# Performance work log

Hardware: AMD Instinct MI355X
Metric: run time of the kernel (lower is better)

The kernel has to match this reference:

```python
import jax, jax.numpy as jnp
import numpy as np

EPS = 1e-5  # torch LayerNorm default


def _lstm_layer(x, Wih, Whh, bih, bhh):
    """Batched multi-weight LSTM layer.
    x: (N, T, I); Wih: (N, 4H, I); Whh: (N, 4H, H); bih, bhh: (N, 4H).
    Gate order matches PyTorch: i, f, g, o.
    Returns (hs: (N, T, H), h_last: (N, H)).
    """
    N, T, _ = x.shape
    H = Whh.shape[-1]
    # Precompute input projections for all timesteps (high-intensity GEMM).
    xW = jnp.einsum('nti,ngi->ntg', x, Wih) + (bih + bhh)[:, None, :]  # (N, T, 4H)

    def step(carry, xt):
        h, c = carry
        gates = xt + jnp.einsum('nh,ngh->ng', h, Whh)  # (N, 4H)
        i, f, g, o = jnp.split(gates, 4, axis=-1)
        i = jax.nn.sigmoid(i)
        f = jax.nn.sigmoid(f)
        g = jnp.tanh(g)
        o = jax.nn.sigmoid(o)
        c = f * c + i * g
        h = o * jnp.tanh(c)
        return (h, c), h

    h0 = jnp.zeros((N, H), dtype=x.dtype)
    c0 = jnp.zeros((N, H), dtype=x.dtype)
    (h_last, _), hs = jax.lax.scan(step, (h0, c0), jnp.swapaxes(xW, 0, 1))
    return jnp.swapaxes(hs, 0, 1), h_last


def _layer_norm(x, gamma, beta):
    mu = jnp.mean(x, axis=-1, keepdims=True)
    var = jnp.mean(jnp.square(x - mu), axis=-1, keepdims=True)
    return (x - mu) * jax.lax.rsqrt(var + EPS) * gamma + beta


def setup_inputs() -> dict:
    key = jax.random.key(0)
    N, T, I, H = 128, 512, 32, 256
    ks = jax.random.split(key, 10)
    k = 1.0 / np.sqrt(H)  # torch LSTM init scale
    u = lambda kk, shape: jax.random.uniform(kk, shape, jnp.float32, -k, k)
    return {
        'x': jax.random.normal(ks[0], (N, T, I), jnp.float32),
        # layer 0 (input I -> H)
        'Wih0': u(ks[1], (N, 4 * H, I)),
        'Whh0': u(ks[2], (N, 4 * H, H)),
        'bih0': u(ks[3], (N, 4 * H)),
        'bhh0': u(ks[4], (N, 4 * H)),
        # layer 1 (H -> H)
        'Wih1': u(ks[5], (N, 4 * H, H)),
        'Whh1': u(ks[6], (N, 4 * H, H)),
        'bih1': u(ks[7], (N, 4 * H)),
        'bhh1': u(ks[8], (N, 4 * H)),
        # LayerNorm params
        'gamma': jnp.ones((H,), jnp.float32),
        'beta': jnp.zeros((H,), jnp.float32),
    }


def reference(x, Wih0, Whh0, bih0, bhh0, Wih1, Whh1, bih1, bhh1, gamma, beta):
    # Eval-mode forward: Dropout layers are identity.
    hs0, _ = _lstm_layer(x, Wih0, Whh0, bih0, bhh0)      # (N, T, H)
    _, h_last = _lstm_layer(hs0, Wih1, Whh1, bih1, bhh1)  # (N, H) = top-layer final hidden state
    return _layer_norm(h_last, gamma, beta)               # (N, H)
```

## Files before the change

kernel.cpp:

```cpp
#include <hip/hip_runtime.h>
#include <hip/hip_bf16.h>


typedef _Float16 half2_t __attribute__((ext_vector_type(2)));
typedef _Float16 half8_t __attribute__((ext_vector_type(8)));
typedef float floatx4 __attribute__((ext_vector_type(4)));

__device__ __forceinline__ unsigned pk(float a, float b) {
  half2_t h = { (_Float16)a, (_Float16)b };
  return __builtin_bit_cast(unsigned, h);
}
__device__ __forceinline__ float fdot2(unsigned w, unsigned h, float c) {
  return __builtin_amdgcn_fdot2(__builtin_bit_cast(half2_t, w),
                                __builtin_bit_cast(half2_t, h), c, false);
}
__device__ __forceinline__ float h2f(unsigned short u) {
  return (float)__builtin_bit_cast(_Float16, u);
}
__device__ __forceinline__ unsigned short f2h(float f) {
  return __builtin_bit_cast(unsigned short, (_Float16)f);
}
__device__ __forceinline__ float sigmf(float x) {
  return __builtin_amdgcn_rcpf(1.f + __expf(-x));
}
__device__ __forceinline__ float tanh_(float x) {
  return 2.f * sigmf(2.f * x) - 1.f;
}
__device__ __forceinline__ floatx4 mfma16(half8_t a, half8_t b, floatx4 c) {
  return __builtin_amdgcn_mfma_f32_16x16x32_f16(a, b, c, 0, 0, 0);
}

template<int K, int KT, bool AF16>
__global__ __launch_bounds__(256)
void gemm_xw(const void* __restrict__ Ap, const float* __restrict__ Bp,
             unsigned short* __restrict__ Cp)
{
  __shared__ unsigned short As[128][KT + 8];
  __shared__ unsigned short Bs[128][KT + 8];
  const int tid = threadIdx.x;
  const int node = blockIdx.y;
  const int mt = blockIdx.x >> 3;
  const int nt = blockIdx.x & 7;
  const int lane = tid & 63, wv = tid >> 6;
  const int wr = wv >> 1, wc = wv & 1;
  const int lm = lane & 15, lk = (lane >> 4) * 8;

  floatx4 zero = {0.f, 0.f, 0.f, 0.f};
  floatx4 acc[4][4];
#pragma unroll
  for (int i = 0; i < 4; ++i)
#pragma unroll
    for (int j = 0; j < 4; ++j) acc[i][j] = zero;

  for (int kt = 0; kt < K; kt += KT) {
    if (AF16) {
      const unsigned short* A = (const unsigned short*)Ap + (size_t)node * 512 * K;
      const int CPR = KT / 8;
#pragma unroll
      for (int c = tid; c < 128 * CPR; c += 256) {
        int r = c / CPR, cc = (c % CPR) * 8;
        *(uint4*)&As[r][cc] =
            *(const uint4*)(A + (size_t)(mt * 128 + r) * K + kt + cc);
      }
    } else {
      const float* A = (const float*)Ap + (size_t)node * 512 * K;
      const int CPR = KT / 4;
#pragma unroll
      for (int c = tid; c < 128 * CPR; c += 256) {
        int r = c / CPR, cc = (c % CPR) * 4;
        float4 v = *(const float4*)(A + (size_t)(mt * 128 + r) * K + kt + cc);
        uint2 p = make_uint2(pk(v.x, v.y), pk(v.z, v.w));
        *(uint2*)&As[r][cc] = p;
      }
    }
    {
      const float* B = Bp + (size_t)node * 1024 * K;
      const int CPR = KT / 4;
#pragma unroll
      for (int c = tid; c < 128 * CPR; c += 256) {
        int r = c / CPR, cc = (c % CPR) * 4;
        float4 v = *(const float4*)(B + (size_t)(nt * 128 + r) * K + kt + cc);
        uint2 p = make_uint2(pk(v.x, v.y), pk(v.z, v.w));
        *(uint2*)&Bs[r][cc] = p;
      }
    }
    __syncthreads();
#pragma unroll
    for (int ks = 0; ks < KT / 32; ++ks) {
      half8_t af[4], bf[4];
#pragma unroll
      for (int i = 0; i < 4; ++i)
        af[i] = *(const half8_t*)&As[wr * 64 + i * 16 + lm][ks * 32 + lk];
#pragma unroll
      for (int j = 0; j < 4; ++j)
        bf[j] = *(const half8_t*)&Bs[wc * 64 + j * 16 + lm][ks * 32 + lk];
#pragma unroll
      for (int i = 0; i < 4; ++i)
#pragma unroll
        for (int j = 0; j < 4; ++j)
          acc[i][j] = mfma16(af[i], bf[j], acc[i][j]);
    }
    __syncthreads();
  }
  unsigned short* C = Cp + (size_t)node * 512 * 1024;
#pragma unroll
  for (int i = 0; i < 4; ++i)
#pragma unroll
    for (int j = 0; j < 4; ++j)
#pragma unroll
      for (int r = 0; r < 4; ++r) {
        int row = mt * 128 + wr * 64 + i * 16 + (lane >> 4) * 4 + r;
        int col = nt * 128 + wc * 64 + j * 16 + lm;
        C[(size_t)row * 1024 + col] = f2h(acc[i][j][r]);
      }
}

#define VWP 96

template<bool WRITE_HS, bool FINAL>
__global__ __launch_bounds__(512, 2)
void lstm_rec(const unsigned short* __restrict__ xW,
              const float* __restrict__ Whh,
              const float* __restrict__ bih, const float* __restrict__ bhh,
              unsigned* __restrict__ hs,
              const float* __restrict__ gamma, const float* __restrict__ beta,
              float* __restrict__ out)
{
  __shared__ uint4 lw4[16][512];
  __shared__ __align__(16) unsigned short hbuf[256];
  __shared__ float fBuf[256], oBuf[256];
  __shared__ float redBuf[2];

  const int tid = threadIdx.x;
  const int n = blockIdx.x;
  const int g0 = tid, g1 = tid + 512;

  const float b0 = bih[n * 1024 + g0] + bhh[n * 1024 + g0];
  const float b1 = bih[n * 1024 + g1] + bhh[n * 1024 + g1];

  const float4* w0p = (const float4*)(Whh + ((size_t)n * 1024 + g0) * 256);
  const float4* w1p = (const float4*)(Whh + ((size_t)n * 1024 + g1) * 256);
  unsigned wv0[VWP], wv1[VWP];
#pragma unroll
  for (int i = 0; i < VWP / 2; ++i) {
    float4 v = w0p[i];
    wv0[2 * i] = pk(v.x, v.y);
    wv0[2 * i + 1] = pk(v.z, v.w);
    float4 u = w1p[i];
    wv1[2 * i] = pk(u.x, u.y);
    wv1[2 * i + 1] = pk(u.z, u.w);
  }
#pragma unroll
  for (int i = 0; i < 8; ++i) {
    float4 a = w0p[48 + 2 * i], b = w0p[49 + 2 * i];
    lw4[i][tid] = make_uint4(pk(a.x, a.y), pk(a.z, a.w), pk(b.x, b.y), pk(b.z, b.w));
    float4 c4 = w1p[48 + 2 * i], d4 = w1p[49 + 2 * i];
    lw4[8 + i][tid] = make_uint4(pk(c4.x, c4.y), pk(c4.z, c4.w), pk(d4.x, d4.y), pk(d4.z, d4.w));
  }

  if (tid < 32) ((uint4*)hbuf)[tid] = make_uint4(0, 0, 0, 0);
  float c = 0.f, hl = 0.f;
  const unsigned short* xwp = xW + (size_t)n * 512 * 1024;
  __syncthreads();

  for (int t = 0; t < 512; ++t) {
    unsigned short xu0 = xwp[t * 1024 + g0];
    unsigned short xu1 = xwp[t * 1024 + g1];
    float a0 = b0, a1 = b1;
    const uint4* h4 = (const uint4*)hbuf;
#pragma unroll
    for (int q = 0; q < 24; ++q) {
      uint4 hp = h4[q];
      a0 = fdot2(wv0[4 * q + 0], hp.x, a0); a1 = fdot2(wv1[4 * q + 0], hp.x, a1);
      a0 = fdot2(wv0[4 * q + 1], hp.y, a0); a1 = fdot2(wv1[4 * q + 1], hp.y, a1);
      a0 = fdot2(wv0[4 * q + 2], hp.z, a0); a1 = fdot2(wv1[4 * q + 2], hp.z, a1);
      a0 = fdot2(wv0[4 * q + 3], hp.w, a0); a1 = fdot2(wv1[4 * q + 3], hp.w, a1);
    }
#pragma unroll
    for (int q = 0; q < 8; ++q) {
      uint4 hp = h4[24 + q];
      uint4 u0 = lw4[q][tid], u1 = lw4[8 + q][tid];
      a0 = fdot2(u0.x, hp.x, a0); a1 = fdot2(u1.x, hp.x, a1);
      a0 = fdot2(u0.y, hp.y, a0); a1 = fdot2(u1.y, hp.y, a1);
      a0 = fdot2(u0.z, hp.z, a0); a1 = fdot2(u1.z, hp.z, a1);
      a0 = fdot2(u0.w, hp.w, a0); a1 = fdot2(u1.w, hp.w, a1);
    }
    a0 += h2f(xu0);
    a1 += h2f(xu1);

    float iact = 0.f, gact = 0.f;
    if (tid < 256) {
      iact = sigmf(a0);
      gact = tanh_(a1);
    } else {
      fBuf[tid - 256] = sigmf(a0);
      oBuf[tid - 256] = sigmf(a1);
    }
    __syncthreads();
    if (tid < 256) {
      c = fBuf[tid] * c + iact * gact;
      hl = oBuf[tid] * tanh_(c);
      hbuf[tid] = f2h(hl);
    }
    __syncthreads();
    if (WRITE_HS && tid < 128)
      hs[((size_t)n * 512 + t) * 128 + tid] = ((const unsigned*)hbuf)[tid];
  }

  if (FINAL) {
    if (tid < 256) fBuf[tid] = hl;
    __syncthreads();
    if (tid < 64) {
      float s = fBuf[tid] + fBuf[tid + 64] + fBuf[tid + 128] + fBuf[tid + 192];
      for (int off = 32; off > 0; off >>= 1) s += __shfl_down(s, off, 64);
      if (tid == 0) redBuf[0] = s * (1.f / 256.f);
    }
    __syncthreads();
    float mu = redBuf[0];
    if (tid < 256) oBuf[tid] = (hl - mu) * (hl - mu);
    __syncthreads();
    if (tid < 64) {
      float s = oBuf[tid] + oBuf[tid + 64] + oBuf[tid + 128] + oBuf[tid + 192];
      for (int off = 32; off > 0; off >>= 1) s += __shfl_down(s, off, 64);
      if (tid == 0) redBuf[1] = s * (1.f / 256.f);
    }
    __syncthreads();
    if (tid < 256) {
      float var = redBuf[1];
      out[(size_t)n * 256 + tid] =
          (hl - mu) * rsqrtf(var + 1e-5f) * gamma[tid] + beta[tid];
    }
  }
}

extern "C" void kernel_launch(void* const* d_in, const int* in_sizes, int n_in,
                              void* d_out, int out_size, void* d_ws, size_t ws_size,
                              hipStream_t stream) {
  const float* x     = (const float*)d_in[0];
  const float* Wih0  = (const float*)d_in[1];
  const float* Whh0  = (const float*)d_in[2];
  const float* bih0  = (const float*)d_in[3];
  const float* bhh0  = (const float*)d_in[4];
  const float* Wih1  = (const float*)d_in[5];
  const float* Whh1  = (const float*)d_in[6];
  const float* bih1  = (const float*)d_in[7];
  const float* bhh1  = (const float*)d_in[8];
  const float* gamma = (const float*)d_in[9];
  const float* beta  = (const float*)d_in[10];
  float* out = (float*)d_out;

  unsigned short* xw  = (unsigned short*)d_ws;
  unsigned short* hs0 = (unsigned short*)((char*)d_ws + (size_t)134217728);

  gemm_xw<32, 32, false><<<dim3(32, 128), 256, 0, stream>>>(x, Wih0, xw);
  lstm_rec<true, false><<<128, 512, 0, stream>>>(xw, Whh0, bih0, bhh0,
                                                 (unsigned*)hs0, nullptr, nullptr,
                                                 nullptr);
  gemm_xw<256, 128, true><<<dim3(32, 128), 256, 0, stream>>>(hs0, Wih1, xw);
  lstm_rec<false, true><<<128, 512, 0, stream>>>(xw, Whh1, bih1, bhh1, nullptr,
                                                 gamma, beta, out);
}
```

Measured before the change: 2.469 ms.

## Restructure LSTM recurrence: 256 threads, split-K across lane quads with DPP reduction

```diff
diff --git a/kernel.cpp b/kernel.cpp
--- a/kernel.cpp
+++ b/kernel.cpp
@@ -28,6 +28,12 @@
 }
 __device__ __forceinline__ floatx4 mfma16(half8_t a, half8_t b, floatx4 c) {
   return __builtin_amdgcn_mfma_f32_16x16x32_f16(a, b, c, 0, 0, 0);
+}
+template<int CTRL>
+__device__ __forceinline__ float dppf(float x) {
+  return __builtin_bit_cast(
+      float, __builtin_amdgcn_update_dpp(0, __builtin_bit_cast(int, x), CTRL,
+                                         0xf, 0xf, true));
 }
 
 template<int K, int KT, bool AF16>
@@ -115,121 +121,131 @@
       }
 }
 
-#define VWP 96
-
 template<bool WRITE_HS, bool FINAL>
-__global__ __launch_bounds__(512, 2)
+__global__ __launch_bounds__(256, 1)
 void lstm_rec(const unsigned short* __restrict__ xW,
               const float* __restrict__ Whh,
               const float* __restrict__ bih, const float* __restrict__ bhh,
-              unsigned* __restrict__ hs,
+              unsigned short* __restrict__ hs,
               const float* __restrict__ gamma, const float* __restrict__ beta,
               float* __restrict__ out)
 {
-  __shared__ uint4 lw4[16][512];
-  __shared__ __align__(16) unsigned short hbuf[256];
-  __shared__ float fBuf[256], oBuf[256];
-  __shared__ float redBuf[2];
+  __shared__ uint4 lwL[16][2][256];
+  __shared__ __align__(16) unsigned short hbuf[2][256];
+  __shared__ float red[256];
+  __shared__ float redv[2];
 
   const int tid = threadIdx.x;
   const int n = blockIdx.x;
-  const int g0 = tid, g1 = tid + 512;
-
-  const float b0 = bih[n * 1024 + g0] + bhh[n * 1024 + g0];
-  const float b1 = bih[n * 1024 + g1] + bhh[n * 1024 + g1];
-
-  const float4* w0p = (const float4*)(Whh + ((size_t)n * 1024 + g0) * 256);
-  const float4* w1p = (const float4*)(Whh + ((size_t)n * 1024 + g1) * 256);
-  unsigned wv0[VWP], wv1[VWP];
-#pragma unroll
-  for (int i = 0; i < VWP / 2; ++i) {
-    float4 v = w0p[i];
-    wv0[2 * i] = pk(v.x, v.y);
-    wv0[2 * i + 1] = pk(v.z, v.w);
-    float4 u = w1p[i];
-    wv1[2 * i] = pk(u.x, u.y);
-    wv1[2 * i + 1] = pk(u.z, u.w);
-  }
-#pragma unroll
-  for (int i = 0; i < 8; ++i) {
-    float4 a = w0p[48 + 2 * i], b = w0p[49 + 2 * i];
-    lw4[i][tid] = make_uint4(pk(a.x, a.y), pk(a.z, a.w), pk(b.x, b.y), pk(b.z, b.w));
-    float4 c4 = w1p[48 + 2 * i], d4 = w1p[49 + 2 * i];
-    lw4[8 + i][tid] = make_uint4(pk(c4.x, c4.y), pk(c4.z, c4.w), pk(d4.x, d4.y), pk(d4.z, d4.w));
-  }
-
-  if (tid < 32) ((uint4*)hbuf)[tid] = make_uint4(0, 0, 0, 0);
+  const int l = tid & 63, w = tid >> 6;
+  const int r = l & 3;
+  const int u0 = w * 64 + (l >> 2) * 4;
+  const int u = w * 64 + l;
+
+  float bias[4];
+#pragma unroll
+  for (int G = 0; G < 4; ++G)
+    bias[G] = bih[n * 1024 + G * 256 + u] + bhh[n * 1024 + G * 256 + u];
+
+  unsigned wv[16 * 24];
+#pragma unroll
+  for (int G = 0; G < 4; ++G)
+#pragma unroll
+    for (int j = 0; j < 4; ++j) {
+      const int s = G * 4 + j;
+      const int row = G * 256 + u0 + ((r + j) & 3);
+      const float4* Wp =
+          (const float4*)(Whh + ((size_t)n * 1024 + row) * 256 + 64 * r);
+#pragma unroll
+      for (int m = 0; m < 12; ++m) {
+        float4 v = Wp[m];
+        wv[s * 24 + 2 * m]     = pk(v.x, v.y);
+        wv[s * 24 + 2 * m + 1] = pk(v.z, v.w);
+      }
+      float4 a = Wp[12], b = Wp[13];
+      lwL[s][0][tid] = make_uint4(pk(a.x, a.y), pk(a.z, a.w), pk(b.x, b.y), pk(b.z, b.w));
+      float4 c4 = Wp[14], d4 = Wp[15];
+      lwL[s][1][tid] = make_uint4(pk(c4.x, c4.y), pk(c4.z, c4.w), pk(d4.x, d4.y), pk(d4.z, d4.w));
+    }
+
+  hbuf[0][tid] = 0;
   float c = 0.f, hl = 0.f;
   const unsigned short* xwp = xW + (size_t)n * 512 * 1024;
   __syncthreads();
 
   for (int t = 0; t < 512; ++t) {
-    unsigned short xu0 = xwp[t * 1024 + g0];
-    unsigned short xu1 = xwp[t * 1024 + g1];
-    float a0 = b0, a1 = b1;
-    const uint4* h4 = (const uint4*)hbuf;
-#pragma unroll
-    for (int q = 0; q < 24; ++q) {
-      uint4 hp = h4[q];
-      a0 = fdot2(wv0[4 * q + 0], hp.x, a0); a1 = fdot2(wv1[4 * q + 0], hp.x, a1);
-      a0 = fdot2(wv0[4 * q + 1], hp.y, a0); a1 = fdot2(wv1[4 * q + 1], hp.y, a1);
-      a0 = fdot2(wv0[4 * q + 2], hp.z, a0); a1 = fdot2(wv1[4 * q + 2], hp.z, a1);
-      a0 = fdot2(wv0[4 * q + 3], hp.w, a0); a1 = fdot2(wv1[4 * q + 3], hp.w, a1);
-    }
-#pragma unroll
-    for (int q = 0; q < 8; ++q) {
-      uint4 hp = h4[24 + q];
-      uint4 u0 = lw4[q][tid], u1 = lw4[8 + q][tid];
-      a0 = fdot2(u0.x, hp.x, a0); a1 = fdot2(u1.x, hp.x, a1);
-      a0 = fdot2(u0.y, hp.y, a0); a1 = fdot2(u1.y, hp.y, a1);
-      a0 = fdot2(u0.z, hp.z, a0); a1 = fdot2(u1.z, hp.z, a1);
-      a0 = fdot2(u0.w, hp.w, a0); a1 = fdot2(u1.w, hp.w, a1);
-    }
-    a0 += h2f(xu0);
-    a1 += h2f(xu1);
-
-    float iact = 0.f, gact = 0.f;
-    if (tid < 256) {
-      iact = sigmf(a0);
-      gact = tanh_(a1);
-    } else {
-      fBuf[tid - 256] = sigmf(a0);
-      oBuf[tid - 256] = sigmf(a1);
-    }
-    __syncthreads();
-    if (tid < 256) {
-      c = fBuf[tid] * c + iact * gact;
-      hl = oBuf[tid] * tanh_(c);
-      hbuf[tid] = f2h(hl);
-    }
-    __syncthreads();
-    if (WRITE_HS && tid < 128)
-      hs[((size_t)n * 512 + t) * 128 + tid] = ((const unsigned*)hbuf)[tid];
+    const int p = t & 1, np = p ^ 1;
+    unsigned short xv0 = xwp[t * 1024 + 0 * 256 + u];
+    unsigned short xv1 = xwp[t * 1024 + 1 * 256 + u];
+    unsigned short xv2 = xwp[t * 1024 + 2 * 256 + u];
+    unsigned short xv3 = xwp[t * 1024 + 3 * 256 + u];
+
+    unsigned hd[32];
+    {
+      const uint4* hb = (const uint4*)(&hbuf[p][64 * r]);
+#pragma unroll
+      for (int m = 0; m < 8; ++m) {
+        uint4 q = hb[m];
+        hd[4 * m] = q.x; hd[4 * m + 1] = q.y; hd[4 * m + 2] = q.z; hd[4 * m + 3] = q.w;
+      }
+    }
+
+    float acc[16];
+#pragma unroll
+    for (int s = 0; s < 16; ++s) {
+      float a = 0.f;
+#pragma unroll
+      for (int d = 0; d < 24; ++d) a = fdot2(wv[s * 24 + d], hd[d], a);
+      uint4 t0 = lwL[s][0][tid];
+      a = fdot2(t0.x, hd[24], a); a = fdot2(t0.y, hd[25], a);
+      a = fdot2(t0.z, hd[26], a); a = fdot2(t0.w, hd[27], a);
+      uint4 t1 = lwL[s][1][tid];
+      a = fdot2(t1.x, hd[28], a); a = fdot2(t1.y, hd[29], a);
+      a = fdot2(t1.z, hd[30], a); a = fdot2(t1.w, hd[31], a);
+      acc[s] = a;
+    }
+
+    float A0 = acc[0] + dppf<0x93>(acc[1]) + dppf<0x4E>(acc[2]) + dppf<0x39>(acc[3]);
+    float A1 = acc[4] + dppf<0x93>(acc[5]) + dppf<0x4E>(acc[6]) + dppf<0x39>(acc[7]);
+    float A2 = acc[8] + dppf<0x93>(acc[9]) + dppf<0x4E>(acc[10]) + dppf<0x39>(acc[11]);
+    float A3 = acc[12] + dppf<0x93>(acc[13]) + dppf<0x4E>(acc[14]) + dppf<0x39>(acc[15]);
+
+    A0 += bias[0] + h2f(xv0);
+    A1 += bias[1] + h2f(xv1);
+    A2 += bias[2] + h2f(xv2);
+    A3 += bias[3] + h2f(xv3);
+
+    float iv = sigmf(A0), fv = sigmf(A1), gv = tanh_(A2), ov = sigmf(A3);
+    c = fv * c + iv * gv;
+    hl = ov * tanh_(c);
+    unsigned short hh = f2h(hl);
+    hbuf[np][u] = hh;
+    if (WRITE_HS)
+      hs[((size_t)n * 512 + t) * 256 + u] = hh;
+    __syncthreads();
   }
 
   if (FINAL) {
-    if (tid < 256) fBuf[tid] = hl;
+    red[tid] = hl;
     __syncthreads();
     if (tid < 64) {
-      float s = fBuf[tid] + fBuf[tid + 64] + fBuf[tid + 128] + fBuf[tid + 192];
+      float s = red[tid] + red[tid + 64] + red[tid + 128] + red[tid + 192];
       for (int off = 32; off > 0; off >>= 1) s += __shfl_down(s, off, 64);
-      if (tid == 0) redBuf[0] = s * (1.f / 256.f);
-    }
-    __syncthreads();
-    float mu = redBuf[0];
-    if (tid < 256) oBuf[tid] = (hl - mu) * (hl - mu);
+      if (tid == 0) redv[0] = s * (1.f / 256.f);
+    }
+    __syncthreads();
+    float mu = redv[0];
+    red[tid] = (hl - mu) * (hl - mu);
     __syncthreads();
     if (tid < 64) {
-      float s = oBuf[tid] + oBuf[tid + 64] + oBuf[tid + 128] + oBuf[tid + 192];
+      float s = red[tid] + red[tid + 64] + red[tid + 128] + red[tid + 192];
       for (int off = 32; off > 0; off >>= 1) s += __shfl_down(s, off, 64);
-      if (tid == 0) redBuf[1] = s * (1.f / 256.f);
-    }
-    __syncthreads();
-    if (tid < 256) {
-      float var = redBuf[1];
-      out[(size_t)n * 256 + tid] =
-          (hl - mu) * rsqrtf(var + 1e-5f) * gamma[tid] + beta[tid];
-    }
+      if (tid == 0) redv[1] = s * (1.f / 256.f);
+    }
+    __syncthreads();
+    float var = redv[1];
+    out[(size_t)n * 256 + u] =
+        (hl - mu) * rsqrtf(var + 1e-5f) * gamma[u] + beta[u];
   }
 }
 
@@ -253,10 +269,9 @@
   unsigned short* hs0 = (unsigned short*)((char*)d_ws + (size_t)134217728);
 
   gemm_xw<32, 32, false><<<dim3(32, 128), 256, 0, stream>>>(x, Wih0, xw);
-  lstm_rec<true, false><<<128, 512, 0, stream>>>(xw, Whh0, bih0, bhh0,
-                                                 (unsigned*)hs0, nullptr, nullptr,
-                                                 nullptr);
+  lstm_rec<true, false><<<128, 256, 0, stream>>>(xw, Whh0, bih0, bhh0, hs0,
+                                                 nullptr, nullptr, nullptr);
   gemm_xw<256, 128, true><<<dim3(32, 128), 256, 0, stream>>>(hs0, Wih1, xw);
-  lstm_rec<false, true><<<128, 512, 0, stream>>>(xw, Whh1, bih1, bhh1, nullptr,
+  lstm_rec<false, true><<<128, 256, 0, stream>>>(xw, Whh1, bih1, bhh1, nullptr,
                                                  gamma, beta, out);
 }
```

Result: slower. 3.961 ms (+60.4%).
